# Kernel tuning notes

Measured on AMD Instinct MI355X. Metric: run time of the kernel, lower is better.

Reference implementation:

```python
import jax, jax.numpy as jnp
import numpy as np

B, N, T, K = 2, 128, 1000, 30
L, S, R, DC = 4, 12, 8, 4  # layers, d_state, dt_rank, d_conv


def _ln(x, w, b, eps=1e-5):
    m = jnp.mean(x, -1, keepdims=True)
    v = jnp.var(x, -1, keepdims=True)
    return (x - m) * jax.lax.rsqrt(v + eps) * w + b


def setup_inputs():
    key = jax.random.key(0)
    ks = jax.random.split(key, 10)
    n = lambda k, shp, s=0.05: jax.random.normal(k, shp, jnp.float32) * s
    return {
        "x": jax.random.normal(ks[0], (B, N, T, K), jnp.float32),
        "ln_w": jnp.ones((L, N), jnp.float32),
        "ln_b": jnp.zeros((L, N), jnp.float32),
        "in_w": n(ks[1], (L, 2 * N, N)),
        "in_b": jnp.zeros((L, 2 * N), jnp.float32),
        "conv_w": n(ks[2], (L, N, DC), 0.3),
        "conv_b": jnp.zeros((L, N), jnp.float32),
        "xp_w": n(ks[3], (L, R + 2 * S, N)),
        "dtp_w": n(ks[4], (L, N, R)),
        "dtp_b": n(ks[5], (L, N), 0.5),
        "A_log": jnp.log(jnp.tile(jnp.arange(1.0, S + 1.0, dtype=jnp.float32), (L, N, 1))),
        "Dv": jnp.ones((L, N), jnp.float32),
        "out_w": n(ks[6], (L, N, N)),
        "out_b": jnp.zeros((L, N), jnp.float32),
        "cb_w": n(ks[7], (N, N), 0.09),
        "cb_b": jnp.zeros((N,), jnp.float32),
        "cb_ln_w": jnp.ones((N,), jnp.float32),
        "cb_ln_b": jnp.zeros((N,), jnp.float32),
        "fin_ln_w": jnp.ones((N,), jnp.float32),
        "fin_ln_b": jnp.zeros((N,), jnp.float32),
    }


def _mamba_block(seq, p):
    # seq: [BK, T, N]; canonical Mamba-1 block with pre-LN and residual
    lnw, lnb, iw, ib, cw, cb, xw, dw, db, alog, dv, ow, ob = p
    x = _ln(seq, lnw, lnb)
    xz = x @ iw.T + ib                         # [BK,T,2N]
    xc, z = jnp.split(xz, 2, axis=-1)
    # causal depthwise conv, kernel size DC
    xp = jnp.pad(xc, ((0, 0), (DC - 1, 0), (0, 0)))
    Tlen = xc.shape[1]
    conv = sum(xp[:, k:k + Tlen, :] * cw[:, k] for k in range(DC))
    xc = jax.nn.silu(conv + cb)
    dbc = xc @ xw.T                            # [BK,T,R+2S]
    dt = jax.nn.softplus(dbc[..., :R] @ dw.T + db)  # [BK,T,N]
    Bm = dbc[..., R:R + S]                     # [BK,T,S]
    Cm = dbc[..., R + S:]                      # [BK,T,S]
    A = -jnp.exp(alog)                         # [N,S]

    def step(h, inp):
        dt_t, B_t, C_t, x_t = inp              # [BK,N],[BK,S],[BK,S],[BK,N]
        dA = jnp.exp(dt_t[..., None] * A)      # [BK,N,S]
        h = dA * h + dt_t[..., None] * B_t[:, None, :] * x_t[..., None]
        y = jnp.einsum('bns,bs->bn', h, C_t)
        return h, y

    h0 = jnp.zeros((xc.shape[0], xc.shape[2], S), xc.dtype)
    xs = (jnp.swapaxes(dt, 0, 1), jnp.swapaxes(Bm, 0, 1),
          jnp.swapaxes(Cm, 0, 1), jnp.swapaxes(xc, 0, 1))
    _, ys = jax.lax.scan(step, h0, xs)
    y = jnp.swapaxes(ys, 0, 1) + dv * xc
    y = y * jax.nn.silu(z)
    return y @ ow.T + ob + seq


def reference(x, ln_w, ln_b, in_w, in_b, conv_w, conv_b, xp_w, dtp_w, dtp_b,
              A_log, Dv, out_w, out_b, cb_w, cb_b, cb_ln_w, cb_ln_b, fin_ln_w, fin_ln_b):
    b, n, t, k = x.shape
    seq = jnp.transpose(x, (0, 3, 2, 1)).reshape(b * k, t, n)  # [BK,T,N]

    def lstep(s, p):
        return _mamba_block(s, p), None

    seq, _ = jax.lax.scan(lstep, seq, (ln_w, ln_b, in_w, in_b, conv_w, conv_b,
                                       xp_w, dtp_w, dtp_b, A_log, Dv, out_w, out_b))
    main = jnp.transpose(seq.reshape(b, k, t, n), (0, 2, 1, 3))  # [B,T,K,N]
    cross = jax.nn.gelu(_ln(main @ cb_w.T + cb_b, cb_ln_w, cb_ln_b), approximate=False)
    feat = _ln(main + cross, fin_ln_w, fin_ln_b)
    return jnp.transpose(feat, (0, 3, 1, 2))  # [B,N,T,K]
```

## Files before the change

kernel.cpp:

```cpp
#include <hip/hip_runtime.h>
#include <math.h>

#define BKS 60
#define TL  1000
#define NF  128
#define SD  12
#define RD  8
#define NCH 32
#define CLEN 32
#define NTOK (BKS*TL)
#define MT  64
#define NBLK ((NTOK + MT - 1)/MT)
#define LNP 129
#define OFF_OW  131072
#define OFF_CBW 196608
#define OFF_XW  212992
#define WCNT    229376

typedef __bf16 bf16x8 __attribute__((ext_vector_type(8)));
typedef float  f32x4  __attribute__((ext_vector_type(4)));

__device__ __forceinline__ float siluf(float x){ return x / (1.f + __expf(-x)); }
__device__ __forceinline__ float softplusf(float x){
  if (x > 20.f) return x;
  float e = __expf(x);
  return (x < -20.f) ? e : __logf(1.f + e);
}
__device__ __forceinline__ ushort bf16r(float f){
  uint u = __float_as_uint(f);
  return (ushort)((u + 0x7FFFu + ((u>>16)&1u)) >> 16);
}
__device__ __forceinline__ float bf2f(ushort h){ return __uint_as_float(((uint)h)<<16); }

__global__ __launch_bounds__(256) void k_ingest(const float* __restrict__ x, float* __restrict__ seq){
  const int b = blockIdx.x / TL, t = blockIdx.x % TL;
  __shared__ float tile[30*NF];
  for (int e = threadIdx.x; e < 30*NF; e += 256){
    int n = e / 30, k = e - n*30;
    tile[k*NF + n] = x[((size_t)(b*NF + n)*TL + t)*30 + k];
  }
  __syncthreads();
  const size_t base = ((size_t)b*30)*TL*NF + (size_t)t*NF;
  for (int e = threadIdx.x; e < 30*NF; e += 256){
    int k = e >> 7, n = e & 127;
    seq[base + (size_t)k*TL*NF + n] = tile[e];
  }
}

__global__ __launch_bounds__(256) void k_wconv(
    const float* __restrict__ iw, const float* __restrict__ ow,
    const float* __restrict__ cw, const float* __restrict__ xw,
    ushort* __restrict__ wh, ushort* __restrict__ wl){
  const int idx = blockIdx.x*256 + threadIdx.x;
  if (idx >= WCNT) return;
  float v;
  if (idx < OFF_OW)       v = iw[idx];
  else if (idx < OFF_CBW) v = ow[idx - OFF_OW];
  else if (idx < OFF_XW)  v = cw[idx - OFF_CBW];
  else                    v = xw[idx - OFF_XW];
  const ushort h = bf16r(v);
  wh[idx] = h;
  wl[idx] = bf16r(v - bf2f(h));
}

__global__ __launch_bounds__(256) void k_ln_inproj(
    const float* __restrict__ seq, const float* __restrict__ lnw, const float* __restrict__ lnb,
    const ushort* __restrict__ wh, const ushort* __restrict__ wl, const float* __restrict__ ib,
    float* __restrict__ xcr, float* __restrict__ zb){
  __shared__ short xsh[MT*NF];
  __shared__ short xsl[MT*NF];
  const int tid = threadIdx.x;
  const int tok0 = blockIdx.x * MT;

  {
    const int j = tid >> 4, l16 = tid & 15;
    for (int it = 0; it < 4; ++it){
      const int t = j + 16*it;
      const int tok = tok0 + t;
      float v[8]; float s = 0.f, s2 = 0.f;
      if (tok < NTOK){
        const float* sp = seq + (size_t)tok*NF;
        #pragma unroll
        for (int i = 0; i < 8; ++i){ float f = sp[l16 + 16*i]; v[i] = f; s += f; s2 += f*f; }
      } else {
        #pragma unroll
        for (int i = 0; i < 8; ++i) v[i] = 0.f;
      }
      #pragma unroll
      for (int m = 1; m < 16; m <<= 1){ s += __shfl_xor(s, m, 64); s2 += __shfl_xor(s2, m, 64); }
      const float mean = s * (1.f/128.f);
      const float rstd = rsqrtf(s2*(1.f/128.f) - mean*mean + 1e-5f);
      const int swz = (t & 7) << 3;
      #pragma unroll
      for (int i = 0; i < 8; ++i){
        const int n = l16 + 16*i;
        const float f = (v[i]-mean)*rstd*lnw[n] + lnb[n];
        const ushort h = bf16r(f);
        xsh[t*NF + (n ^ swz)] = (short)h;
        xsl[t*NF + (n ^ swz)] = (short)bf16r(f - bf2f(h));
      }
    }
  }
  __syncthreads();

  const int w = tid >> 6, lane = tid & 63;
  const int cl = lane & 15, q8 = (lane >> 4) * 8;
  const int obase = w * 64;
  f32x4 acc[4][4];
  #pragma unroll
  for (int m = 0; m < 4; ++m)
    #pragma unroll
    for (int nt = 0; nt < 4; ++nt) acc[m][nt] = (f32x4){0.f,0.f,0.f,0.f};

  for (int c = 0; c < 4; ++c){
    bf16x8 ah[4], al[4];
    #pragma unroll
    for (int m = 0; m < 4; ++m){
      const int r = m*16 + cl;
      const int hi = r*NF + ((c*32 + q8) ^ ((r & 7) << 3));
      ah[m] = *(const bf16x8*)&xsh[hi];
      al[m] = *(const bf16x8*)&xsl[hi];
    }
    #pragma unroll
    for (int nt = 0; nt < 4; ++nt){
      const int o = obase + nt*16 + cl;
      const size_t wo = (size_t)o*NF + c*32 + q8;
      const bf16x8 bh = *(const bf16x8*)(wh + wo);
      const bf16x8 bl = *(const bf16x8*)(wl + wo);
      #pragma unroll
      for (int m = 0; m < 4; ++m){
        acc[m][nt] = __builtin_amdgcn_mfma_f32_16x16x32_bf16(ah[m], bh, acc[m][nt], 0, 0, 0);
        acc[m][nt] = __builtin_amdgcn_mfma_f32_16x16x32_bf16(al[m], bh, acc[m][nt], 0, 0, 0);
        acc[m][nt] = __builtin_amdgcn_mfma_f32_16x16x32_bf16(ah[m], bl, acc[m][nt], 0, 0, 0);
      }
    }
  }

  const int rbase = (lane >> 4) * 4;
  #pragma unroll
  for (int nt = 0; nt < 4; ++nt){
    const int o = obase + nt*16 + cl;
    const float bias = ib[o];
    float* dst = (o < NF) ? xcr : zb;
    const int oc = (o < NF) ? o : (o - NF);
    #pragma unroll
    for (int m = 0; m < 4; ++m)
      #pragma unroll
      for (int j2 = 0; j2 < 4; ++j2){
        const int tok = tok0 + m*16 + rbase + j2;
        if (tok < NTOK) dst[(size_t)tok*NF + oc] = acc[m][nt][j2] + bias;
      }
  }
}

__global__ __launch_bounds__(256) void k_conv_scan1(
    const float* __restrict__ xcr,
    const float* __restrict__ cw, const float* __restrict__ cb,
    const ushort* __restrict__ xwh, const ushort* __restrict__ xwl,
    const float* __restrict__ dw, const float* __restrict__ db,
    const float* __restrict__ alog,
    float* __restrict__ xcc, float* __restrict__ dtb,
    float* __restrict__ Bmb, float* __restrict__ Cmb,
    float* __restrict__ ap, float* __restrict__ hfb){
  __shared__ float smem[9600];
  float* sxr  = smem;
  float* sdt  = smem;
  short* xch  = (short*)(smem + 4480);
  short* xcl  = (short*)(smem + 6528);
  float* sdbc = smem + 8576;
  const int bid = blockIdx.x;
  const int sq = bid / NCH, cblk = bid - sq*NCH;
  const int t0 = cblk*CLEN;
  const int lim = (TL - t0 < CLEN) ? (TL - t0) : CLEN;
  const int tid = threadIdx.x;

  for (int i = 0; i < 5; ++i){
    const int e4 = tid + i*256;
    if (e4 < 35*32){
      const int r = e4 >> 5, n4 = (e4 & 31) << 2;
      const int t = t0 - 3 + r;
      float4 v = make_float4(0.f,0.f,0.f,0.f);
      if (t >= 0 && t < TL) v = *(const float4*)(xcr + ((size_t)sq*TL + t)*NF + n4);
      *(float4*)(sxr + r*NF + n4) = v;
    }
  }
  __syncthreads();

  #pragma unroll
  for (int i = 0; i < 4; ++i){
    const int e4 = tid + i*256;
    const int r = e4 >> 5, n4 = (e4 & 31) << 2;
    const float4 c0 = *(const float4*)(cw + (size_t)(n4+0)*4);
    const float4 c1 = *(const float4*)(cw + (size_t)(n4+1)*4);
    const float4 c2 = *(const float4*)(cw + (size_t)(n4+2)*4);
    const float4 c3 = *(const float4*)(cw + (size_t)(n4+3)*4);
    const float4 x0 = *(const float4*)(sxr + (r+0)*NF + n4);
    const float4 x1 = *(const float4*)(sxr + (r+1)*NF + n4);
    const float4 x2 = *(const float4*)(sxr + (r+2)*NF + n4);
    const float4 x3 = *(const float4*)(sxr + (r+3)*NF + n4);
    float4 a = *(const float4*)(cb + n4);
    a.x = fmaf(x3.x, c0.w, fmaf(x2.x, c0.z, fmaf(x1.x, c0.y, fmaf(x0.x, c0.x, a.x))));
    a.y = fmaf(x3.y, c1.w, fmaf(x2.y, c1.z, fmaf(x1.y, c1.y, fmaf(x0.y, c1.x, a.y))));
    a.z = fmaf(x3.z, c2.w, fmaf(x2.z, c2.z, fmaf(x1.z, c2.y, fmaf(x0.z, c2.x, a.z))));
    a.w = fmaf(x3.w, c3.w, fmaf(x2.w, c3.z, fmaf(x1.w, c3.y, fmaf(x0.w, c3.x, a.w))));
    a.x = siluf(a.x); a.y = siluf(a.y); a.z = siluf(a.z); a.w = siluf(a.w);
    const ushort h0 = bf16r(a.x), h1 = bf16r(a.y), h2 = bf16r(a.z), h3 = bf16r(a.w);
    const ushort l0 = bf16r(a.x - bf2f(h0)), l1 = bf16r(a.y - bf2f(h1));
    const ushort l2 = bf16r(a.z - bf2f(h2)), l3 = bf16r(a.w - bf2f(h3));
    const int bi = r*NF + (n4 ^ ((r & 7) << 3));
    *(uint2*)&xch[bi] = make_uint2((uint)h0 | ((uint)h1 << 16), (uint)h2 | ((uint)h3 << 16));
    *(uint2*)&xcl[bi] = make_uint2((uint)l0 | ((uint)l1 << 16), (uint)l2 | ((uint)l3 << 16));
    if (r < lim) *(float4*)(xcc + ((size_t)sq*TL + t0 + r)*NF + n4) = a;
  }
  __syncthreads();

  {
    const int w = tid >> 6, lane = tid & 63;
    const int cl = lane & 15, q8 = (lane >> 4) * 8;
    const int m = w & 1, nt = w >> 1;
    f32x4 acc = (f32x4){0.f,0.f,0.f,0.f};
    for (int c = 0; c < 4; ++c){
      const int r = m*16 + cl;
      const int ai = r*NF + ((c*32 + q8) ^ ((r & 7) << 3));
      const bf16x8 ah = *(const bf16x8*)&xch[ai];
      const bf16x8 al = *(const bf16x8*)&xcl[ai];
      const int o = nt*16 + cl;
      const size_t wo = (size_t)o*NF + c*32 + q8;
      const bf16x8 bh = *(const bf16x8*)(xwh + wo);
      const bf16x8 bl = *(const bf16x8*)(xwl + wo);
      acc = __builtin_amdgcn_mfma_f32_16x16x32_bf16(ah, bh, acc, 0, 0, 0);
      acc = __builtin_amdgcn_mfma_f32_16x16x32_bf16(al, bh, acc, 0, 0, 0);
      acc = __builtin_amdgcn_mfma_f32_16x16x32_bf16(ah, bl, acc, 0, 0, 0);
    }
    const int rb = m*16 + (lane >> 4)*4;
    const int o = nt*16 + cl;
    #pragma unroll
    for (int j = 0; j < 4; ++j)
      sdbc[(rb + j)*32 + o] = acc[j];
  }
  __syncthreads();

  #pragma unroll
  for (int i = 0; i < 16; ++i){
    const int e = tid + i*256;
    const int r = e >> 7, n = e & 127;
    const float4 b0 = *(const float4*)(sdbc + r*32);
    const float4 b1 = *(const float4*)(sdbc + r*32 + 4);
    const float4 w0 = *(const float4*)(dw + (size_t)n*8);
    const float4 w1 = *(const float4*)(dw + (size_t)n*8 + 4);
    float acc = db[n];
    acc = fmaf(b0.x, w0.x, acc); acc = fmaf(b0.y, w0.y, acc);
    acc = fmaf(b0.z, w0.z, acc); acc = fmaf(b0.w, w0.w, acc);
    acc = fmaf(b1.x, w1.x, acc); acc = fmaf(b1.y, w1.y, acc);
    acc = fmaf(b1.z, w1.z, acc); acc = fmaf(b1.w, w1.w, acc);
    const float dtv = softplusf(acc);
    sdt[e] = dtv;
    if (e < lim*NF) dtb[((size_t)sq*TL + t0)*NF + e] = dtv;
  }
  for (int e = tid; e < CLEN*2*SD; e += 256){
    int r = e / (2*SD), c = e - r*2*SD;
    if (r < lim){
      float v = sdbc[r*32 + 8 + c];
      size_t tok = (size_t)sq*TL + t0 + r;
      if (c < SD) Bmb[tok*SD + c] = v;
      else        Cmb[tok*SD + (c - SD)] = v;
    }
  }
  __syncthreads();

  {
    const int n = tid & 127, p = tid >> 7;
    float Av[6], h[6];
    #pragma unroll
    for (int s = 0; s < 6; ++s){
      Av[s] = -__expf(alog[(size_t)n*SD + p*6 + s]);
      h[s] = 0.f;
    }
    bool fast = true;
    #pragma unroll
    for (int s = 0; s < 6; ++s)
      fast = fast && (fabsf(Av[s] + (float)(p*6 + s + 1)) <= 1e-3f);
    float dts = 0.f;
    if (fast){
      for (int tt = 0; tt < lim; ++tt){
        const float dtv = sdt[tt*NF + n];
        const int xi = tt*NF + (n ^ ((tt & 7) << 3));
        const float xcv = bf2f((ushort)xch[xi]) + bf2f((ushort)xcl[xi]);
        float Bv[6];
        const float* br = sdbc + tt*32 + 8 + p*6;
        if (p == 0){
          const float4 a = *(const float4*)br;
          const float2 b = *(const float2*)(br + 4);
          Bv[0]=a.x; Bv[1]=a.y; Bv[2]=a.z; Bv[3]=a.w; Bv[4]=b.x; Bv[5]=b.y;
        } else {
          const float2 a = *(const float2*)br;
          const float4 b = *(const float4*)(br + 2);
          Bv[0]=a.x; Bv[1]=a.y; Bv[2]=b.x; Bv[3]=b.y; Bv[4]=b.z; Bv[5]=b.w;
        }
        const float dx = dtv * xcv;
        dts += dtv;
        const float q = __expf(-dtv);
        float dA;
        if (p == 0) dA = q;
        else { const float q2 = q*q; const float q4 = q2*q2; dA = q4*q2*q; }
        h[0] = fmaf(dA, h[0], dx*Bv[0]);
        #pragma unroll
        for (int s = 1; s < 6; ++s){ dA *= q; h[s] = fmaf(dA, h[s], dx*Bv[s]); }
      }
    } else {
      for (int tt = 0; tt < lim; ++tt){
        const float dtv = sdt[tt*NF + n];
        const int xi = tt*NF + (n ^ ((tt & 7) << 3));
        const float xcv = bf2f((ushort)xch[xi]) + bf2f((ushort)xcl[xi]);
        float Bv[6];
        const float* br = sdbc + tt*32 + 8 + p*6;
        if (p == 0){
          const float4 a = *(const float4*)br;
          const float2 b = *(const float2*)(br + 4);
          Bv[0]=a.x; Bv[1]=a.y; Bv[2]=a.z; Bv[3]=a.w; Bv[4]=b.x; Bv[5]=b.y;
        } else {
          const float2 a = *(const float2*)br;
          const float4 b = *(const float4*)(br + 2);
          Bv[0]=a.x; Bv[1]=a.y; Bv[2]=b.x; Bv[3]=b.y; Bv[4]=b.z; Bv[5]=b.w;
        }
        const float dx = dtv * xcv;
        dts += dtv;
        #pragma unroll
        for (int s = 0; s < 6; ++s){
          const float dA = __expf(dtv*Av[s]);
          h[s] = fmaf(dA, h[s], dx*Bv[s]);
        }
      }
    }
    const size_t base = (size_t)bid*SD*NF + n;
    #pragma unroll
    for (int s = 0; s < 6; ++s){
      ap [base + (p*6+s)*NF] = __expf(Av[s]*dts);
      hfb[base + (p*6+s)*NF] = h[s];
    }
  }
}

__global__ __launch_bounds__(128) void k_scan_combine(
    const float* __restrict__ ap, const float* __restrict__ hfb, float* __restrict__ hinit){
  const int sq = blockIdx.x;
  const int n = threadIdx.x;
  float h[SD];
  #pragma unroll
  for (int s = 0; s < SD; ++s) h[s] = 0.f;
  for (int c = 0; c < NCH; ++c){
    const size_t base = ((size_t)sq*NCH + c)*SD*NF + n;
    #pragma unroll
    for (int s = 0; s < SD; ++s){
      hinit[base + s*NF] = h[s];
      h[s] = fmaf(ap[base + s*NF], h[s], hfb[base + s*NF]);
    }
  }
}

__global__ __launch_bounds__(128) void k_scan_pass2(
    const float* __restrict__ dtb, const float* __restrict__ xcc,
    const float* __restrict__ Bmb, const float* __restrict__ Cmb,
    const float* __restrict__ alog, const float* __restrict__ hinit,
    const float* __restrict__ zb, const float* __restrict__ Dv,
    float* __restrict__ yb){
  const int bid = blockIdx.x;
  const int sq = bid / NCH, c = bid - sq*NCH;
  const int t0 = c*CLEN;
  const int lim = (TL - t0 < CLEN) ? (TL - t0) : CLEN;
  const int n = threadIdx.x;
  const float4* A4 = (const float4*)(alog + (size_t)n*SD);
  float4 Aa = A4[0], Ab = A4[1], Ac = A4[2];
  float Av[SD] = {Aa.x,Aa.y,Aa.z,Aa.w, Ab.x,Ab.y,Ab.z,Ab.w, Ac.x,Ac.y,Ac.z,Ac.w};
  #pragma unroll
  for (int s = 0; s < SD; ++s) Av[s] = -__expf(Av[s]);
  bool fast = true;
  #pragma unroll
  for (int s = 0; s < SD; ++s)
    fast = fast && (fabsf(Av[s] + (float)(s + 1)) <= 1e-3f);
  const float dvn = Dv[n];
  float h[SD];
  const size_t hbase = (size_t)bid*SD*NF + n;
  #pragma unroll
  for (int s = 0; s < SD; ++s) h[s] = hinit[hbase + s*NF];
  const size_t tok0 = (size_t)sq*TL + t0;
  if (fast){
    for (int tt = 0; tt < lim; ++tt){
      const size_t tok = tok0 + tt;
      float dtv = dtb[tok*NF + n];
      float xcv = xcc[tok*NF + n];
      float dx  = dtv * xcv;
      const float4* B4 = (const float4*)(Bmb + tok*SD);
      const float4* C4 = (const float4*)(Cmb + tok*SD);
      float4 Ba=B4[0], Bb=B4[1], Bc=B4[2];
      float4 Ca=C4[0], Cb=C4[1], Cc=C4[2];
      float Bv[SD] = {Ba.x,Ba.y,Ba.z,Ba.w, Bb.x,Bb.y,Bb.z,Bb.w, Bc.x,Bc.y,Bc.z,Bc.w};
      float Cv[SD] = {Ca.x,Ca.y,Ca.z,Ca.w, Cb.x,Cb.y,Cb.z,Cb.w, Cc.x,Cc.y,Cc.z,Cc.w};
      const float q = __expf(-dtv);
      float dA = q;
      float yv = 0.f;
      h[0] = fmaf(dA, h[0], dx*Bv[0]);
      yv = fmaf(h[0], Cv[0], yv);
      #pragma unroll
      for (int s = 1; s < SD; ++s){
        dA *= q;
        h[s] = fmaf(dA, h[s], dx*Bv[s]);
        yv = fmaf(h[s], Cv[s], yv);
      }
      float zv = zb[tok*NF + n];
      yb[tok*NF + n] = fmaf(dvn, xcv, yv) * siluf(zv);
    }
  } else {
    for (int tt = 0; tt < lim; ++tt){
      const size_t tok = tok0 + tt;
      float dtv = dtb[tok*NF + n];
      float xcv = xcc[tok*NF + n];
      float dx  = dtv * xcv;
      const float4* B4 = (const float4*)(Bmb + tok*SD);
      const float4* C4 = (const float4*)(Cmb + tok*SD);
      float4 Ba=B4[0], Bb=B4[1], Bc=B4[2];
      float4 Ca=C4[0], Cb=C4[1], Cc=C4[2];
      float Bv[SD] = {Ba.x,Ba.y,Ba.z,Ba.w, Bb.x,Bb.y,Bb.z,Bb.w, Bc.x,Bc.y,Bc.z,Bc.w};
      float Cv[SD] = {Ca.x,Ca.y,Ca.z,Ca.w, Cb.x,Cb.y,Cb.z,Cb.w, Cc.x,Cc.y,Cc.z,Cc.w};
      float yv = 0.f;
      #pragma unroll
      for (int s = 0; s < SD; ++s){
        float dA = __expf(dtv*Av[s]);
        h[s] = fmaf(dA, h[s], dx*Bv[s]);
        yv = fmaf(h[s], Cv[s], yv);
      }
      float zv = zb[tok*NF + n];
      yb[tok*NF + n] = fmaf(dvn, xcv, yv) * siluf(zv);
    }
  }
}

__global__ __launch_bounds__(256) void k_gate_out(
    const float* __restrict__ yb,
    const ushort* __restrict__ wh, const ushort* __restrict__ wl, const float* __restrict__ ob,
    float* __restrict__ seq){
  __shared__ short xsh[MT*NF];
  __shared__ short xsl[MT*NF];
  const int tid = threadIdx.x;
  const int tok0 = blockIdx.x * MT;

  #pragma unroll
  for (int i = 0; i < 8; ++i){
    const int r  = (tid & 15) + ((i & 3) << 4);
    const int nq = (tid >> 4) + ((i >> 2) << 4);
    const int tok = tok0 + r;
    float4 v = make_float4(0.f,0.f,0.f,0.f);
    if (tok < NTOK) v = *(const float4*)(yb + (size_t)tok*NF + nq*4);
    const ushort h0 = bf16r(v.x), h1 = bf16r(v.y), h2 = bf16r(v.z), h3 = bf16r(v.w);
    const ushort l0 = bf16r(v.x - bf2f(h0)), l1 = bf16r(v.y - bf2f(h1));
    const ushort l2 = bf16r(v.z - bf2f(h2)), l3 = bf16r(v.w - bf2f(h3));
    const int hi = r*NF + ((nq*4) ^ ((r & 7) << 3));
    *(uint2*)&xsh[hi] = make_uint2((uint)h0 | ((uint)h1 << 16), (uint)h2 | ((uint)h3 << 16));
    *(uint2*)&xsl[hi] = make_uint2((uint)l0 | ((uint)l1 << 16), (uint)l2 | ((uint)l3 << 16));
  }
  __syncthreads();

  const int w = tid >> 6, lane = tid & 63;
  const int cl = lane & 15, q8 = (lane >> 4) * 8;
  const int obase = w * 32;
  f32x4 acc[4][2];
  #pragma unroll
  for (int m = 0; m < 4; ++m)
    #pragma unroll
    for (int nt = 0; nt < 2; ++nt) acc[m][nt] = (f32x4){0.f,0.f,0.f,0.f};

  for (int c = 0; c < 4; ++c){
    bf16x8 ah[4], al[4];
    #pragma unroll
    for (int m = 0; m < 4; ++m){
      const int r = m*16 + cl;
      const int hi = r*NF + ((c*32 + q8) ^ ((r & 7) << 3));
      ah[m] = *(const bf16x8*)&xsh[hi];
      al[m] = *(const bf16x8*)&xsl[hi];
    }
    #pragma unroll
    for (int nt = 0; nt < 2; ++nt){
      const int o = obase + nt*16 + cl;
      const size_t wo = (size_t)o*NF + c*32 + q8;
      const bf16x8 bh = *(const bf16x8*)(wh + wo);
      const bf16x8 bl = *(const bf16x8*)(wl + wo);
      #pragma unroll
      for (int m = 0; m < 4; ++m){
        acc[m][nt] = __builtin_amdgcn_mfma_f32_16x16x32_bf16(ah[m], bh, acc[m][nt], 0, 0, 0);
        acc[m][nt] = __builtin_amdgcn_mfma_f32_16x16x32_bf16(al[m], bh, acc[m][nt], 0, 0, 0);
        acc[m][nt] = __builtin_amdgcn_mfma_f32_16x16x32_bf16(ah[m], bl, acc[m][nt], 0, 0, 0);
      }
    }
  }

  const int rbase = (lane >> 4) * 4;
  #pragma unroll
  for (int nt = 0; nt < 2; ++nt){
    const int o = obase + nt*16 + cl;
    const float bias = ob[o];
    #pragma unroll
    for (int m = 0; m < 4; ++m)
      #pragma unroll
      for (int j2 = 0; j2 < 4; ++j2){
        const int tok = tok0 + m*16 + rbase + j2;
        if (tok < NTOK){
          float* dst = seq + (size_t)tok*NF + o;
          *dst = *dst + acc[m][nt][j2] + bias;
        }
      }
  }
}

__global__ __launch_bounds__(256) void k_cross_gemm(
    const float* __restrict__ seq,
    const ushort* __restrict__ wh, const ushort* __restrict__ wl, const float* __restrict__ cbb,
    float* __restrict__ cross){
  __shared__ short xsh[MT*NF];
  __shared__ short xsl[MT*NF];
  const int tid = threadIdx.x;
  const int tok0 = blockIdx.x * MT;

  #pragma unroll
  for (int i = 0; i < 8; ++i){
    const int r  = (tid & 15) + ((i & 3) << 4);
    const int nq = (tid >> 4) + ((i >> 2) << 4);
    const int tok = tok0 + r;
    float4 v = make_float4(0.f,0.f,0.f,0.f);
    if (tok < NTOK){
      int b = tok / 30000, rr = tok - b*30000;
      int t = rr / 30, k = rr - t*30;
      v = *(const float4*)(seq + ((size_t)(b*30 + k)*TL + t)*NF + nq*4);
    }
    const ushort h0 = bf16r(v.x), h1 = bf16r(v.y), h2 = bf16r(v.z), h3 = bf16r(v.w);
    const ushort l0 = bf16r(v.x - bf2f(h0)), l1 = bf16r(v.y - bf2f(h1));
    const ushort l2 = bf16r(v.z - bf2f(h2)), l3 = bf16r(v.w - bf2f(h3));
    const int hi = r*NF + ((nq*4) ^ ((r & 7) << 3));
    *(uint2*)&xsh[hi] = make_uint2((uint)h0 | ((uint)h1 << 16), (uint)h2 | ((uint)h3 << 16));
    *(uint2*)&xsl[hi] = make_uint2((uint)l0 | ((uint)l1 << 16), (uint)l2 | ((uint)l3 << 16));
  }
  __syncthreads();

  const int w = tid >> 6, lane = tid & 63;
  const int cl = lane & 15, q8 = (lane >> 4) * 8;
  const int obase = w * 32;
  f32x4 acc[4][2];
  #pragma unroll
  for (int m = 0; m < 4; ++m)
    #pragma unroll
    for (int nt = 0; nt < 2; ++nt) acc[m][nt] = (f32x4){0.f,0.f,0.f,0.f};

  for (int c = 0; c < 4; ++c){
    bf16x8 ah[4], al[4];
    #pragma unroll
    for (int m = 0; m < 4; ++m){
      const int r = m*16 + cl;
      const int hi = r*NF + ((c*32 + q8) ^ ((r & 7) << 3));
      ah[m] = *(const bf16x8*)&xsh[hi];
      al[m] = *(const bf16x8*)&xsl[hi];
    }
    #pragma unroll
    for (int nt = 0; nt < 2; ++nt){
      const int o = obase + nt*16 + cl;
      const size_t wo = (size_t)o*NF + c*32 + q8;
      const bf16x8 bh = *(const bf16x8*)(wh + wo);
      const bf16x8 bl = *(const bf16x8*)(wl + wo);
      #pragma unroll
      for (int m = 0; m < 4; ++m){
        acc[m][nt] = __builtin_amdgcn_mfma_f32_16x16x32_bf16(ah[m], bh, acc[m][nt], 0, 0, 0);
        acc[m][nt] = __builtin_amdgcn_mfma_f32_16x16x32_bf16(al[m], bh, acc[m][nt], 0, 0, 0);
        acc[m][nt] = __builtin_amdgcn_mfma_f32_16x16x32_bf16(ah[m], bl, acc[m][nt], 0, 0, 0);
      }
    }
  }

  const int rbase = (lane >> 4) * 4;
  #pragma unroll
  for (int nt = 0; nt < 2; ++nt){
    const int o = obase + nt*16 + cl;
    const float bias = cbb[o];
    #pragma unroll
    for (int m = 0; m < 4; ++m)
      #pragma unroll
      for (int j2 = 0; j2 < 4; ++j2){
        const int tok = tok0 + m*16 + rbase + j2;
        if (tok < NTOK) cross[(size_t)tok*NF + o] = acc[m][nt][j2] + bias;
      }
  }
}

__global__ __launch_bounds__(256) void k_cross_ln(
    const float* __restrict__ seq, const float* __restrict__ cross,
    const float* __restrict__ clnw, const float* __restrict__ clnb,
    const float* __restrict__ flnw, const float* __restrict__ flnb,
    float* __restrict__ out){
  __shared__ float fs[32*LNP];
  const int tid = threadIdx.x;
  const int tok0 = blockIdx.x * 32;
  const int j16 = tid >> 4, l16 = tid & 15;

  for (int it = 0; it < 2; ++it){
    const int jj = j16 + 16*it;
    const int tok = tok0 + jj;
    const int b = tok / 30000, rr = tok - b*30000;
    const int t = rr / 30, k = rr - t*30;
    const float* cp = cross + (size_t)tok*NF;
    const float* mp = seq + ((size_t)(b*30 + k)*TL + t)*NF;
    float cv[8]; float s = 0.f, s2 = 0.f;
    #pragma unroll
    for (int i = 0; i < 8; ++i){
      float f = cp[l16 + 16*i]; cv[i] = f; s += f; s2 += f*f;
    }
    #pragma unroll
    for (int m = 1; m < 16; m <<= 1){ s += __shfl_xor(s, m, 64); s2 += __shfl_xor(s2, m, 64); }
    float mu = s * (1.f/128.f);
    float rs = rsqrtf(s2*(1.f/128.f) - mu*mu + 1e-5f);
    float rv[8]; float rsum = 0.f, rsum2 = 0.f;
    #pragma unroll
    for (int i = 0; i < 8; ++i){
      int n = l16 + 16*i;
      float cn = (cv[i] - mu)*rs*clnw[n] + clnb[n];
      float g = 0.5f*cn*(1.f + erff(cn*0.70710678118f));
      float res = mp[n] + g;
      rv[i] = res; rsum += res; rsum2 += res*res;
    }
    #pragma unroll
    for (int m = 1; m < 16; m <<= 1){ rsum += __shfl_xor(rsum, m, 64); rsum2 += __shfl_xor(rsum2, m, 64); }
    float mu2 = rsum * (1.f/128.f);
    float rs2 = rsqrtf(rsum2*(1.f/128.f) - mu2*mu2 + 1e-5f);
    #pragma unroll
    for (int i = 0; i < 8; ++i){
      int n = l16 + 16*i;
      fs[jj*LNP + n] = (rv[i] - mu2)*rs2*flnw[n] + flnb[n];
    }
  }
  __syncthreads();

  #pragma unroll
  for (int i = 0; i < 16; ++i){
    const int e = tid + i*256;
    const int j = e & 31, n = e >> 5;
    const int tok = tok0 + j;
    const int b = tok / 30000, rr = tok - b*30000;
    out[(size_t)(b*NF + n)*30000 + rr] = fs[j*LNP + n];
  }
}

extern "C" void kernel_launch(void* const* d_in, const int* in_sizes, int n_in,
                              void* d_out, int out_size, void* d_ws, size_t ws_size,
                              hipStream_t stream){
  const float* x       = (const float*)d_in[0];
  const float* ln_w    = (const float*)d_in[1];
  const float* ln_b    = (const float*)d_in[2];
  const float* in_w    = (const float*)d_in[3];
  const float* in_b    = (const float*)d_in[4];
  const float* conv_w  = (const float*)d_in[5];
  const float* conv_b  = (const float*)d_in[6];
  const float* xp_w    = (const float*)d_in[7];
  const float* dtp_w   = (const float*)d_in[8];
  const float* dtp_b   = (const float*)d_in[9];
  const float* A_log   = (const float*)d_in[10];
  const float* Dv      = (const float*)d_in[11];
  const float* out_w   = (const float*)d_in[12];
  const float* out_b   = (const float*)d_in[13];
  const float* cb_w    = (const float*)d_in[14];
  const float* cb_b    = (const float*)d_in[15];
  const float* cb_ln_w = (const float*)d_in[16];
  const float* cb_ln_b = (const float*)d_in[17];
  const float* fin_ln_w= (const float*)d_in[18];
  const float* fin_ln_b= (const float*)d_in[19];
  float* out = (float*)d_out;

  const size_t SEQSZ = (size_t)BKS*TL*NF;
  const size_t CHSZ  = (size_t)BKS*NF*NCH*SD;
  const size_t FBASE = 6*SEQSZ + 2*(size_t)BKS*TL*SD;
  const size_t BASE  = FBASE + WCNT;
  float* ws  = (float*)d_ws;
  float* seq = ws;
  float* xcr = ws + SEQSZ;
  float* zb  = ws + 2*SEQSZ;
  float* xcc = ws + 3*SEQSZ;
  float* dtb = ws + 4*SEQSZ;
  float* yb  = ws + 5*SEQSZ;
  float* Bmb = ws + 6*SEQSZ;
  float* Cmb = Bmb + (size_t)BKS*TL*SD;
  ushort* wbh = (ushort*)(ws + FBASE);
  ushort* wbl = wbh + WCNT;
  if (ws_size < BASE*sizeof(float)) return;

  float* ap    = yb;
  float* hfb   = yb + CHSZ;
  float* hinit = xcr;
  float* cross = dtb;

  k_wconv<<<(WCNT + 255)/256, 256, 0, stream>>>(in_w, out_w, cb_w, xp_w, wbh, wbl);
  k_ingest<<<2*TL, 256, 0, stream>>>(x, seq);
  for (int l = 0; l < 4; ++l){
    k_ln_inproj<<<NBLK, 256, 0, stream>>>(seq, ln_w + l*NF, ln_b + l*NF,
        wbh + (size_t)l*32768, wbl + (size_t)l*32768, in_b + l*2*NF, xcr, zb);
    k_conv_scan1<<<BKS*NCH, 256, 0, stream>>>(xcr, conv_w + (size_t)l*NF*4, conv_b + l*NF,
        wbh + OFF_XW + (size_t)l*4096, wbl + OFF_XW + (size_t)l*4096,
        dtp_w + (size_t)l*NF*RD, dtp_b + l*NF,
        A_log + (size_t)l*NF*SD, xcc, dtb, Bmb, Cmb, ap, hfb);
    k_scan_combine<<<BKS, NF, 0, stream>>>(ap, hfb, hinit);
    k_scan_pass2<<<BKS*NCH, NF, 0, stream>>>(dtb, xcc, Bmb, Cmb, A_log + (size_t)l*NF*SD,
        hinit, zb, Dv + l*NF, yb);
    k_gate_out<<<NBLK, 256, 0, stream>>>(yb,
        wbh + OFF_OW + (size_t)l*16384, wbl + OFF_OW + (size_t)l*16384, out_b + l*NF, seq);
  }
  k_cross_gemm<<<NBLK, 256, 0, stream>>>(seq, wbh + OFF_CBW, wbl + OFF_CBW, cb_b, cross);
  k_cross_ln<<<NTOK/32, 256, 0, stream>>>(seq, cross, cb_ln_w, cb_ln_b, fin_ln_w, fin_ln_b, out);
}
```

Measured before the change: 740.6 us.

## Fuse scan second pass into output projection and recompute dt from low-rank projections

Merges the scan pass-2 kernel with the gated output GEMM. Each block now scans two 32-step chunks of one sequence and writes the gated y straight into shared memory as split bf16 hi/lo for the MFMA projection, so the yb buffer no longer goes through global memory. Instead of storing the full 128-wide dt tensor, the first scan kernel stores only the 8-wide dt-rank projections, and the fused kernel recomputes dt with softplus. This cuts global traffic and one launch per layer. The costs are fewer blocks (960 of 256 threads), only 128 lanes per 32-step chunk doing serial work while the MFMA part waits, and redundant dt arithmetic.

```diff
diff --git a/kernel.cpp b/kernel.cpp
--- a/kernel.cpp
+++ b/kernel.cpp
@@ -159,7 +159,7 @@
     const ushort* __restrict__ xwh, const ushort* __restrict__ xwl,
     const float* __restrict__ dw, const float* __restrict__ db,
     const float* __restrict__ alog,
-    float* __restrict__ xcc, float* __restrict__ dtb,
+    float* __restrict__ xcc, float* __restrict__ dcb,
     float* __restrict__ Bmb, float* __restrict__ Cmb,
     float* __restrict__ ap, float* __restrict__ hfb){
   __shared__ float smem[9600];
@@ -253,9 +253,12 @@
     acc = fmaf(b0.z, w0.z, acc); acc = fmaf(b0.w, w0.w, acc);
     acc = fmaf(b1.x, w1.x, acc); acc = fmaf(b1.y, w1.y, acc);
     acc = fmaf(b1.z, w1.z, acc); acc = fmaf(b1.w, w1.w, acc);
-    const float dtv = softplusf(acc);
-    sdt[e] = dtv;
-    if (e < lim*NF) dtb[((size_t)sq*TL + t0)*NF + e] = dtv;
+    sdt[e] = softplusf(acc);
+  }
+  if (tid < 64){
+    const int t = tid >> 1, q = tid & 1;
+    if (t < lim)
+      *(float4*)(dcb + ((size_t)sq*TL + t0 + t)*8 + q*4) = *(const float4*)&sdbc[t*32 + q*4];
   }
   for (int e = tid; e < CLEN*2*SD; e += 256){
     int r = e / (2*SD), c = e - r*2*SD;
@@ -358,105 +361,100 @@
   }
 }
 
-__global__ __launch_bounds__(128) void k_scan_pass2(
-    const float* __restrict__ dtb, const float* __restrict__ xcc,
+__global__ __launch_bounds__(256) void k_back(
+    const float* __restrict__ dcb, const float* __restrict__ xcc,
     const float* __restrict__ Bmb, const float* __restrict__ Cmb,
+    const float* __restrict__ zb,
+    const ushort* __restrict__ wh, const ushort* __restrict__ wl,
+    const float* __restrict__ dw, const float* __restrict__ db,
     const float* __restrict__ alog, const float* __restrict__ hinit,
-    const float* __restrict__ zb, const float* __restrict__ Dv,
-    float* __restrict__ yb){
-  const int bid = blockIdx.x;
-  const int sq = bid / NCH, c = bid - sq*NCH;
-  const int t0 = c*CLEN;
-  const int lim = (TL - t0 < CLEN) ? (TL - t0) : CLEN;
-  const int n = threadIdx.x;
-  const float4* A4 = (const float4*)(alog + (size_t)n*SD);
-  float4 Aa = A4[0], Ab = A4[1], Ac = A4[2];
-  float Av[SD] = {Aa.x,Aa.y,Aa.z,Aa.w, Ab.x,Ab.y,Ab.z,Ab.w, Ac.x,Ac.y,Ac.z,Ac.w};
-  #pragma unroll
-  for (int s = 0; s < SD; ++s) Av[s] = -__expf(Av[s]);
-  bool fast = true;
-  #pragma unroll
-  for (int s = 0; s < SD; ++s)
-    fast = fast && (fabsf(Av[s] + (float)(s + 1)) <= 1e-3f);
-  const float dvn = Dv[n];
-  float h[SD];
-  const size_t hbase = (size_t)bid*SD*NF + n;
-  #pragma unroll
-  for (int s = 0; s < SD; ++s) h[s] = hinit[hbase + s*NF];
-  const size_t tok0 = (size_t)sq*TL + t0;
-  if (fast){
-    for (int tt = 0; tt < lim; ++tt){
-      const size_t tok = tok0 + tt;
-      float dtv = dtb[tok*NF + n];
-      float xcv = xcc[tok*NF + n];
-      float dx  = dtv * xcv;
-      const float4* B4 = (const float4*)(Bmb + tok*SD);
-      const float4* C4 = (const float4*)(Cmb + tok*SD);
-      float4 Ba=B4[0], Bb=B4[1], Bc=B4[2];
-      float4 Ca=C4[0], Cb=C4[1], Cc=C4[2];
-      float Bv[SD] = {Ba.x,Ba.y,Ba.z,Ba.w, Bb.x,Bb.y,Bb.z,Bb.w, Bc.x,Bc.y,Bc.z,Bc.w};
-      float Cv[SD] = {Ca.x,Ca.y,Ca.z,Ca.w, Cb.x,Cb.y,Cb.z,Cb.w, Cc.x,Cc.y,Cc.z,Cc.w};
-      const float q = __expf(-dtv);
-      float dA = q;
-      float yv = 0.f;
-      h[0] = fmaf(dA, h[0], dx*Bv[0]);
-      yv = fmaf(h[0], Cv[0], yv);
-      #pragma unroll
-      for (int s = 1; s < SD; ++s){
-        dA *= q;
-        h[s] = fmaf(dA, h[s], dx*Bv[s]);
-        yv = fmaf(h[s], Cv[s], yv);
-      }
-      float zv = zb[tok*NF + n];
-      yb[tok*NF + n] = fmaf(dvn, xcv, yv) * siluf(zv);
-    }
-  } else {
-    for (int tt = 0; tt < lim; ++tt){
-      const size_t tok = tok0 + tt;
-      float dtv = dtb[tok*NF + n];
-      float xcv = xcc[tok*NF + n];
-      float dx  = dtv * xcv;
-      const float4* B4 = (const float4*)(Bmb + tok*SD);
-      const float4* C4 = (const float4*)(Cmb + tok*SD);
-      float4 Ba=B4[0], Bb=B4[1], Bc=B4[2];
-      float4 Ca=C4[0], Cb=C4[1], Cc=C4[2];
-      float Bv[SD] = {Ba.x,Ba.y,Ba.z,Ba.w, Bb.x,Bb.y,Bb.z,Bb.w, Bc.x,Bc.y,Bc.z,Bc.w};
-      float Cv[SD] = {Ca.x,Ca.y,Ca.z,Ca.w, Cb.x,Cb.y,Cb.z,Cb.w, Cc.x,Cc.y,Cc.z,Cc.w};
-      float yv = 0.f;
-      #pragma unroll
-      for (int s = 0; s < SD; ++s){
-        float dA = __expf(dtv*Av[s]);
-        h[s] = fmaf(dA, h[s], dx*Bv[s]);
-        yv = fmaf(h[s], Cv[s], yv);
-      }
-      float zv = zb[tok*NF + n];
-      yb[tok*NF + n] = fmaf(dvn, xcv, yv) * siluf(zv);
-    }
-  }
-}
-
-__global__ __launch_bounds__(256) void k_gate_out(
-    const float* __restrict__ yb,
-    const ushort* __restrict__ wh, const ushort* __restrict__ wl, const float* __restrict__ ob,
+    const float* __restrict__ Dv, const float* __restrict__ ob,
     float* __restrict__ seq){
   __shared__ short xsh[MT*NF];
   __shared__ short xsl[MT*NF];
+  const int bid = blockIdx.x;
+  const int sq = bid >> 4, cb2 = bid & 15;
+  const int t0 = cb2 * MT;
+  const int lim = (TL - t0 < MT) ? (TL - t0) : MT;
   const int tid = threadIdx.x;
-  const int tok0 = blockIdx.x * MT;
-
-  #pragma unroll
-  for (int i = 0; i < 8; ++i){
-    const int r  = (tid & 15) + ((i & 3) << 4);
-    const int nq = (tid >> 4) + ((i >> 2) << 4);
-    const int tok = tok0 + r;
-    float4 v = make_float4(0.f,0.f,0.f,0.f);
-    if (tok < NTOK) v = *(const float4*)(yb + (size_t)tok*NF + nq*4);
-    const ushort h0 = bf16r(v.x), h1 = bf16r(v.y), h2 = bf16r(v.z), h3 = bf16r(v.w);
-    const ushort l0 = bf16r(v.x - bf2f(h0)), l1 = bf16r(v.y - bf2f(h1));
-    const ushort l2 = bf16r(v.z - bf2f(h2)), l3 = bf16r(v.w - bf2f(h3));
-    const int hi = r*NF + ((nq*4) ^ ((r & 7) << 3));
-    *(uint2*)&xsh[hi] = make_uint2((uint)h0 | ((uint)h1 << 16), (uint)h2 | ((uint)h3 << 16));
-    *(uint2*)&xsl[hi] = make_uint2((uint)l0 | ((uint)l1 << 16), (uint)l2 | ((uint)l3 << 16));
+
+  {
+    const int n = tid & 127, ch = tid >> 7;
+    float Av[SD];
+    {
+      const float4 a0 = *(const float4*)(alog + (size_t)n*SD);
+      const float4 a1 = *(const float4*)(alog + (size_t)n*SD + 4);
+      const float4 a2 = *(const float4*)(alog + (size_t)n*SD + 8);
+      const float t_[SD] = {a0.x,a0.y,a0.z,a0.w, a1.x,a1.y,a1.z,a1.w, a2.x,a2.y,a2.z,a2.w};
+      #pragma unroll
+      for (int s = 0; s < SD; ++s) Av[s] = -__expf(t_[s]);
+    }
+    bool fast = true;
+    #pragma unroll
+    for (int s = 0; s < SD; ++s)
+      fast = fast && (fabsf(Av[s] + (float)(s + 1)) <= 1e-3f);
+    const float4 dw0 = *(const float4*)(dw + (size_t)n*8);
+    const float4 dw1 = *(const float4*)(dw + (size_t)n*8 + 4);
+    const float dbn = db[n];
+    const float dvn = Dv[n];
+    float h[SD];
+    {
+      const size_t hb = ((size_t)(sq*NCH + cb2*2 + ch))*SD*NF + n;
+      #pragma unroll
+      for (int s = 0; s < SD; ++s) h[s] = hinit[hb + s*NF];
+    }
+    int steps = lim - ch*32; if (steps < 0) steps = 0; if (steps > 32) steps = 32;
+    for (int tt = 0; tt < steps; ++tt){
+      const int t = ch*32 + tt;
+      const size_t gt = (size_t)sq*TL + t0 + t;
+      const float4 d0 = *(const float4*)(dcb + gt*8);
+      const float4 d1 = *(const float4*)(dcb + gt*8 + 4);
+      float da = dbn;
+      da = fmaf(d0.x,dw0.x, da); da = fmaf(d0.y,dw0.y, da);
+      da = fmaf(d0.z,dw0.z, da); da = fmaf(d0.w,dw0.w, da);
+      da = fmaf(d1.x,dw1.x, da); da = fmaf(d1.y,dw1.y, da);
+      da = fmaf(d1.z,dw1.z, da); da = fmaf(d1.w,dw1.w, da);
+      const float dtv = softplusf(da);
+      const float xcv = xcc[gt*NF + n];
+      const float zv  = zb [gt*NF + n];
+      const float4 B0 = *(const float4*)(Bmb + gt*SD);
+      const float4 B1 = *(const float4*)(Bmb + gt*SD + 4);
+      const float4 B2 = *(const float4*)(Bmb + gt*SD + 8);
+      const float4 C0 = *(const float4*)(Cmb + gt*SD);
+      const float4 C1 = *(const float4*)(Cmb + gt*SD + 4);
+      const float4 C2 = *(const float4*)(Cmb + gt*SD + 8);
+      const float Bv[SD] = {B0.x,B0.y,B0.z,B0.w, B1.x,B1.y,B1.z,B1.w, B2.x,B2.y,B2.z,B2.w};
+      const float Cv[SD] = {C0.x,C0.y,C0.z,C0.w, C1.x,C1.y,C1.z,C1.w, C2.x,C2.y,C2.z,C2.w};
+      const float dx = dtv * xcv;
+      float yv = 0.f;
+      if (fast){
+        const float q = __expf(-dtv);
+        float dA = q;
+        h[0] = fmaf(dA, h[0], dx*Bv[0]);
+        yv = fmaf(h[0], Cv[0], yv);
+        #pragma unroll
+        for (int s = 1; s < SD; ++s){
+          dA *= q;
+          h[s] = fmaf(dA, h[s], dx*Bv[s]);
+          yv = fmaf(h[s], Cv[s], yv);
+        }
+      } else {
+        #pragma unroll
+        for (int s = 0; s < SD; ++s){
+          const float dA = __expf(dtv*Av[s]);
+          h[s] = fmaf(dA, h[s], dx*Bv[s]);
+          yv = fmaf(h[s], Cv[s], yv);
+        }
+      }
+      const float yf = fmaf(dvn, xcv, yv) * siluf(zv);
+      const ushort hh = bf16r(yf);
+      const int bi = t*NF + (n ^ ((t & 7) << 3));
+      xsh[bi] = (short)hh;
+      xsl[bi] = (short)bf16r(yf - bf2f(hh));
+    }
+  }
+  if (lim < MT){
+    for (int e = tid; e < (MT - lim)*NF; e += 256){ xsh[lim*NF + e] = 0; xsl[lim*NF + e] = 0; }
   }
   __syncthreads();
 
@@ -502,9 +500,9 @@
     for (int m = 0; m < 4; ++m)
       #pragma unroll
       for (int j2 = 0; j2 < 4; ++j2){
-        const int tok = tok0 + m*16 + rbase + j2;
-        if (tok < NTOK){
-          float* dst = seq + (size_t)tok*NF + o;
+        const int lt = m*16 + rbase + j2;
+        if (lt < lim){
+          float* dst = seq + ((size_t)sq*TL + t0 + lt)*NF + o;
           *dst = *dst + acc[m][nt][j2] + bias;
         }
       }
@@ -679,18 +677,18 @@
   float* xcr = ws + SEQSZ;
   float* zb  = ws + 2*SEQSZ;
   float* xcc = ws + 3*SEQSZ;
-  float* dtb = ws + 4*SEQSZ;
-  float* yb  = ws + 5*SEQSZ;
+  float* dcb = ws + 4*SEQSZ;
+  float* scr = ws + 5*SEQSZ;
   float* Bmb = ws + 6*SEQSZ;
   float* Cmb = Bmb + (size_t)BKS*TL*SD;
   ushort* wbh = (ushort*)(ws + FBASE);
   ushort* wbl = wbh + WCNT;
   if (ws_size < BASE*sizeof(float)) return;
 
-  float* ap    = yb;
-  float* hfb   = yb + CHSZ;
+  float* ap    = scr;
+  float* hfb   = scr + CHSZ;
   float* hinit = xcr;
-  float* cross = dtb;
+  float* cross = dcb;
 
   k_wconv<<<(WCNT + 255)/256, 256, 0, stream>>>(in_w, out_w, cb_w, xp_w, wbh, wbl);
   k_ingest<<<2*TL, 256, 0, stream>>>(x, seq);
@@ -700,12 +698,12 @@
     k_conv_scan1<<<BKS*NCH, 256, 0, stream>>>(xcr, conv_w + (size_t)l*NF*4, conv_b + l*NF,
         wbh + OFF_XW + (size_t)l*4096, wbl + OFF_XW + (size_t)l*4096,
         dtp_w + (size_t)l*NF*RD, dtp_b + l*NF,
-        A_log + (size_t)l*NF*SD, xcc, dtb, Bmb, Cmb, ap, hfb);
+        A_log + (size_t)l*NF*SD, xcc, dcb, Bmb, Cmb, ap, hfb);
     k_scan_combine<<<BKS, NF, 0, stream>>>(ap, hfb, hinit);
-    k_scan_pass2<<<BKS*NCH, NF, 0, stream>>>(dtb, xcc, Bmb, Cmb, A_log + (size_t)l*NF*SD,
-        hinit, zb, Dv + l*NF, yb);
-    k_gate_out<<<NBLK, 256, 0, stream>>>(yb,
-        wbh + OFF_OW + (size_t)l*16384, wbl + OFF_OW + (size_t)l*16384, out_b + l*NF, seq);
+    k_back<<<BKS*16, 256, 0, stream>>>(dcb, xcc, Bmb, Cmb, zb,
+        wbh + OFF_OW + (size_t)l*16384, wbl + OFF_OW + (size_t)l*16384,
+        dtp_w + (size_t)l*NF*RD, dtp_b + l*NF,
+        A_log + (size_t)l*NF*SD, hinit, Dv + l*NF, out_b + l*NF, seq);
   }
   k_cross_gemm<<<NBLK, 256, 0, stream>>>(seq, wbh + OFF_CBW, wbl + OFF_CBW, cb_b, cross);
   k_cross_ln<<<NTOK/32, 256, 0, stream>>>(seq, cross, cb_ln_w, cb_ln_b, fin_ln_w, fin_ln_b, out);
```

Result: slower. 861.3 us (+16.3%).
